# Kernel tuning notes

Measured on AMD Instinct MI355X. Metric: run time of the kernel, lower is better.

Reference implementation:

```python
import jax, jax.numpy as jnp
import numpy as np


def setup_inputs() -> dict:
    key = jax.random.key(0)
    ks = jax.random.split(key, 6)
    B, Q, K = 4, 512, 1024
    Dq, Dk, Dv, H = 512, 512, 512, 128
    return {
        "queries": jax.random.normal(ks[0], (B, Q, Dq), dtype=jnp.float32),
        "keys": jax.random.normal(ks[1], (B, K, Dk), dtype=jnp.float32),
        "values": jax.random.normal(ks[2], (B, K, Dv), dtype=jnp.float32),
        "W_q": jax.random.normal(ks[3], (Dq, H), dtype=jnp.float32) / np.sqrt(Dq),
        "W_k": jax.random.normal(ks[4], (Dk, H), dtype=jnp.float32) / np.sqrt(Dk),
        "w_v": jax.random.normal(ks[5], (H,), dtype=jnp.float32) / np.sqrt(H),
    }


def reference(queries, keys, values, W_q, W_k, w_v):
    # Additive (Bahdanau) attention.
    q = jnp.einsum("bqd,dh->bqh", queries, W_q)          # [B,Q,H]
    k = jnp.einsum("bkd,dh->bkh", keys, W_k)             # [B,K,H]
    features = jnp.tanh(q[:, :, None, :] + k[:, None, :, :])  # [B,Q,K,H]
    scores = jnp.einsum("bqkh,h->bqk", features, w_v)    # [B,Q,K]
    attn = jax.nn.softmax(scores, axis=-1)               # [B,Q,K]
    return jnp.einsum("bqk,bkv->bqv", attn, values)      # [B,Q,Dv]
```

## Files before the change

### kernel.cpp

```cpp
#include <hip/hip_runtime.h>

#define BB   4
#define QS   512
#define KSZ  1024
#define DD   512
#define HH   128
#define DVV  512

typedef unsigned int uint;
typedef unsigned short ushort;
typedef __attribute__((ext_vector_type(8)))  short short8;
typedef __attribute__((ext_vector_type(16))) float f32x16;

__device__ __forceinline__ float rcp_fast(float x)  { return __builtin_amdgcn_rcpf(x); }
__device__ __forceinline__ float exp2_fast(float x) { return __builtin_amdgcn_exp2f(x); }

__device__ __forceinline__ void split1(float v, ushort& h, ushort& l) {
    uint u = __float_as_uint(v);
    h = (ushort)(u >> 16);
    float r = v - __uint_as_float(u & 0xffff0000u);
    l = (ushort)(__float_as_uint(r) >> 16);
}

#define NSQ  (BB * QS * DD / 4 / 256)
#define NSK  (BB * KSZ * DD / 4 / 256)
#define NWT  128
#define NVT  (BB * (KSZ / 32) * (DVV / 32))

__global__ __launch_bounds__(256) void split_kernel(
    const float* __restrict__ q, const float* __restrict__ k,
    const float* __restrict__ Wq, const float* __restrict__ Wk,
    const float* __restrict__ val,
    ushort* __restrict__ qh, ushort* __restrict__ ql,
    ushort* __restrict__ kh, ushort* __restrict__ kl,
    ushort* __restrict__ wqh, ushort* __restrict__ wql,
    ushort* __restrict__ wkh, ushort* __restrict__ wkl,
    ushort* __restrict__ vhi, ushort* __restrict__ vlo)
{
    const int id  = blockIdx.x;
    const int tid = threadIdx.x;

    if (id < NSQ + NSK) {
        const float* src; ushort* dh; ushort* dl; size_t i;
        if (id < NSQ) { src = q; dh = qh; dl = ql; i = (size_t)id * 256 + tid; }
        else          { src = k; dh = kh; dl = kl; i = (size_t)(id - NSQ) * 256 + tid; }
        float4 v = ((const float4*)src)[i];
        ushort h0,h1,h2,h3,l0,l1,l2,l3;
        split1(v.x,h0,l0); split1(v.y,h1,l1); split1(v.z,h2,l2); split1(v.w,h3,l3);
        *(ushort4*)&dh[i * 4] = make_ushort4(h0,h1,h2,h3);
        *(ushort4*)&dl[i * 4] = make_ushort4(l0,l1,l2,l3);
        return;
    }
    if (id < NSQ + NSK + NWT) {
        __shared__ float Ts[32][33];
        int t = id - (NSQ + NSK);
        const float* W; ushort* dh; ushort* dl;
        if (t < 64) { W = Wq; dh = wqh; dl = wql; }
        else        { W = Wk; dh = wkh; dl = wkl; t -= 64; }
        const int d0 = (t >> 2) * 32, h0 = (t & 3) * 32;
        {
            const int dd = tid >> 3, c4 = (tid & 7) * 4;
            float4 v = *(const float4*)&W[(size_t)(d0 + dd) * HH + h0 + c4];
            Ts[dd][c4 + 0] = v.x; Ts[dd][c4 + 1] = v.y;
            Ts[dd][c4 + 2] = v.z; Ts[dd][c4 + 3] = v.w;
        }
        __syncthreads();
        {
            const int hh = tid >> 3, d4 = (tid & 7) * 4;
            ushort h[4], l[4];
            #pragma unroll
            for (int i = 0; i < 4; i++) split1(Ts[d4 + i][hh], h[i], l[i]);
            size_t o = (size_t)(h0 + hh) * DD + d0 + d4;
            *(ushort4*)&dh[o] = make_ushort4(h[0], h[1], h[2], h[3]);
            *(ushort4*)&dl[o] = make_ushort4(l[0], l[1], l[2], l[3]);
        }
        return;
    }
    {
        __shared__ float Ts[32][33];
        const int t   = id - (NSQ + NSK + NWT);
        const int b   = t >> 9;
        const int rem = t & 511;
        const int k0  = (rem >> 4) * 32;
        const int n0  = (rem & 15) * 32;
        {
            const int kk = tid >> 3, n4 = (tid & 7) * 4;
            float4 v = *(const float4*)&val[((size_t)b * KSZ + k0 + kk) * DVV + n0 + n4];
            Ts[kk][n4 + 0] = v.x; Ts[kk][n4 + 1] = v.y;
            Ts[kk][n4 + 2] = v.z; Ts[kk][n4 + 3] = v.w;
        }
        __syncthreads();
        {
            const int nn = tid >> 3, k4 = (tid & 7) * 4;
            ushort h[4], l[4];
            #pragma unroll
            for (int i = 0; i < 4; i++) split1(Ts[k4 + i][nn], h[i], l[i]);
            size_t o = ((size_t)b * DVV + n0 + nn) * KSZ + k0 + k4;
            *(ushort4*)&vhi[o] = make_ushort4(h[0], h[1], h[2], h[3]);
            *(ushort4*)&vlo[o] = make_ushort4(l[0], l[1], l[2], l[3]);
        }
    }
}

__global__ __launch_bounds__(256) void proj_mfma_kernel(
    const ushort* __restrict__ qh, const ushort* __restrict__ ql,
    const ushort* __restrict__ kh, const ushort* __restrict__ kl,
    const ushort* __restrict__ wqh, const ushort* __restrict__ wql,
    const ushort* __restrict__ wkh, const ushort* __restrict__ wkl,
    float* __restrict__ eq, float* __restrict__ ek)
{
    const int tid = threadIdx.x, w = tid >> 6, lane = tid & 63;
    const int row = lane & 31, kg = lane >> 5;
    const int gw = blockIdx.x * 4 + w;

    const ushort *pa_h, *pa_l, *pb_h, *pb_l; float* op; int m0, nt;
    if (gw < 256) {
        m0 = (gw >> 2) * 32; nt = gw & 3;
        pa_h = qh; pa_l = ql; pb_h = wqh; pb_l = wql; op = eq;
    } else {
        const int g = gw - 256;
        m0 = (g >> 2) * 32; nt = g & 3;
        pa_h = kh; pa_l = kl; pb_h = wkh; pb_l = wkl; op = ek;
    }

    const ushort* ah_p = pa_h + (size_t)(m0 + row) * DD + kg * 8;
    const ushort* al_p = pa_l + (size_t)(m0 + row) * DD + kg * 8;
    const ushort* bh_p = pb_h + (size_t)(nt * 32 + row) * DD + kg * 8;
    const ushort* bl_p = pb_l + (size_t)(nt * 32 + row) * DD + kg * 8;

    f32x16 acc;
    #pragma unroll
    for (int i = 0; i < 16; i++) acc[i] = 0.f;

    #pragma unroll 4
    for (int ks = 0; ks < DD; ks += 16) {
        short8 ah = *(const short8*)(ah_p + ks);
        short8 al = *(const short8*)(al_p + ks);
        short8 bh = *(const short8*)(bh_p + ks);
        short8 bl = *(const short8*)(bl_p + ks);
        acc = __builtin_amdgcn_mfma_f32_32x32x16_bf16(ah, bh, acc, 0, 0, 0);
        acc = __builtin_amdgcn_mfma_f32_32x32x16_bf16(ah, bl, acc, 0, 0, 0);
        acc = __builtin_amdgcn_mfma_f32_32x32x16_bf16(al, bh, acc, 0, 0, 0);
    }

    const float C2L = 2.8853900817779268f;
    float* ob = op + (size_t)m0 * HH + nt * 32;
    #pragma unroll
    for (int r = 0; r < 16; r++) {
        const int rb = (r & 3) + 8 * (r >> 2) + 4 * kg;
        ob[(size_t)rb * HH + row] = exp2_fast(acc[r] * C2L);
    }
}

__global__ __launch_bounds__(256) void scores_kernel(
    const float* __restrict__ eq, const float* __restrict__ ek,
    const float* __restrict__ wv, ushort* __restrict__ Phi,
    ushort* __restrict__ Plo, float* __restrict__ rsp)
{
    __shared__ float eqs[64][68];
    __shared__ float eks[64][68];

    const int tid = threadIdx.x;
    const int b  = blockIdx.z;
    const int q0 = blockIdx.y * 64;
    const int k0 = blockIdx.x * 64;

    const float* eqb = eq + ((size_t)b * QS  + q0) * HH;
    const float* ekb = ek + ((size_t)b * KSZ + k0) * HH;

    const int tk = tid & 15;
    const int tq = tid >> 4;

    float acc[4][4] = {};

    for (int hc = 0; hc < HH; hc += 64) {
        __syncthreads();
        #pragma unroll
        for (int i = 0; i < 4; i++) {
            int f = tid + i * 256;
            int row = f >> 4, c4 = f & 15;
            *(float4*)&eqs[row][c4 * 4] =
                *(const float4*)&eqb[(size_t)row * HH + hc + c4 * 4];
            *(float4*)&eks[row][c4 * 4] =
                *(const float4*)&ekb[(size_t)row * HH + hc + c4 * 4];
        }
        __syncthreads();

        for (int h0 = 0; h0 < 64; h0 += 4) {
            float4 wv4 = *(const float4*)&wv[hc + h0];
            float4 eq4[4], ek4[4];
            #pragma unroll
            for (int j = 0; j < 4; j++) {
                eq4[j] = *(const float4*)&eqs[tq + 16 * j][h0];
                ek4[j] = *(const float4*)&eks[tk + 16 * j][h0];
            }
            #pragma unroll
            for (int jq = 0; jq < 4; jq++) {
                #pragma unroll
                for (int jk = 0; jk < 4; jk++) {
                    float u0 = fminf(fmaf(eq4[jq].x, ek4[jk].x, 1.0f), 3e7f);
                    float u1 = fminf(fmaf(eq4[jq].y, ek4[jk].y, 1.0f), 3e7f);
                    float u2 = fminf(fmaf(eq4[jq].z, ek4[jk].z, 1.0f), 3e7f);
                    float u3 = fminf(fmaf(eq4[jq].w, ek4[jk].w, 1.0f), 3e7f);
                    float p01 = u0 * u1, p23 = u2 * u3;
                    float n01 = fmaf(wv4.x, u1, wv4.y * u0);
                    float n23 = fmaf(wv4.z, u3, wv4.w * u2);
                    float N = fmaf(n01, p23, n23 * p01);
                    acc[jq][jk] = fmaf(N, rcp_fast(p01 * p23), acc[jq][jk]);
                }
            }
        }
    }

    const float CN = -2.8853900817779268f;
    ushort* ph = Phi + ((size_t)b * QS + q0) * KSZ + k0;
    ushort* pl = Plo + ((size_t)b * QS + q0) * KSZ + k0;
    #pragma unroll
    for (int jq = 0; jq < 4; jq++) {
        float rowp = 0.f;
        #pragma unroll
        for (int jk = 0; jk < 4; jk++) {
            float pv_ = exp2_fast(acc[jq][jk] * CN);
            ushort hh, ll; split1(pv_, hh, ll);
            size_t o = (size_t)(tq + 16 * jq) * KSZ + tk + 16 * jk;
            ph[o] = hh; pl[o] = ll;
            rowp += pv_;
        }
        #pragma unroll
        for (int m = 8; m; m >>= 1) rowp += __shfl_xor(rowp, m);
        if ((tid & 15) == 0)
            rsp[((size_t)b * QS + q0 + tq + 16 * jq) * 16 + blockIdx.x] = rowp;
    }
}

__global__ __launch_bounds__(256) void pv_mfma_kernel(
    const ushort* __restrict__ Phi, const ushort* __restrict__ Plo,
    const ushort* __restrict__ vhi, const ushort* __restrict__ vlo,
    const float* __restrict__ rsp, float* __restrict__ outp)
{
    __shared__ float invs[32];
    __shared__ float accs[2][32][33];

    const int id  = blockIdx.x;
    const int x   = id & 7;
    const int j   = id >> 3;
    const int bm  = x * 8 + (j >> 3);
    const int ntp = j & 7;
    const int b   = bm >> 4, mt = bm & 15;

    const int tid = threadIdx.x, w = tid >> 6, lane = tid & 63;
    const int row = lane & 31, kg = lane >> 5;

    if (tid < 32) {
        const float* rp = rsp + ((size_t)b * QS + mt * 32 + tid) * 16;
        float s = 0.f;
        #pragma unroll
        for (int i = 0; i < 16; i++) s += rp[i];
        invs[tid] = rcp_fast(s);
    }

    const int nt  = ntp * 2 + (w >> 1);
    const int kh0 = (w & 1) * (KSZ / 2);

    const ushort* pah = Phi + ((size_t)b * QS  + mt * 32 + row) * KSZ + kh0 + kg * 8;
    const ushort* pal = Plo + ((size_t)b * QS  + mt * 32 + row) * KSZ + kh0 + kg * 8;
    const ushort* bhp = vhi + ((size_t)b * DVV + nt * 32 + row) * KSZ + kh0 + kg * 8;
    const ushort* blp = vlo + ((size_t)b * DVV + nt * 32 + row) * KSZ + kh0 + kg * 8;

    f32x16 acc;
    #pragma unroll
    for (int i = 0; i < 16; i++) acc[i] = 0.f;

    #pragma unroll 4
    for (int kb = 0; kb < KSZ / 2; kb += 16) {
        short8 ah = *(const short8*)(pah + kb);
        short8 al = *(const short8*)(pal + kb);
        short8 vh = *(const short8*)(bhp + kb);
        short8 vl = *(const short8*)(blp + kb);
        acc = __builtin_amdgcn_mfma_f32_32x32x16_bf16(ah, vh, acc, 0, 0, 0);
        acc = __builtin_amdgcn_mfma_f32_32x32x16_bf16(ah, vl, acc, 0, 0, 0);
        acc = __builtin_amdgcn_mfma_f32_32x32x16_bf16(al, vh, acc, 0, 0, 0);
    }

    if (w & 1) {
        #pragma unroll
        for (int r = 0; r < 16; r++)
            accs[w >> 1][(r & 3) + 8 * (r >> 2) + 4 * kg][row] = acc[r];
    }
    __syncthreads();
    if (!(w & 1)) {
        float* ob = outp + ((size_t)b * QS + mt * 32) * DVV + nt * 32;
        #pragma unroll
        for (int r = 0; r < 16; r++) {
            const int rb = (r & 3) + 8 * (r >> 2) + 4 * kg;
            float v = acc[r] + accs[w >> 1][rb][row];
            ob[(size_t)rb * DVV + row] = v * invs[rb];
        }
    }
}

extern "C" void kernel_launch(void* const* d_in, const int* in_sizes, int n_in,
                              void* d_out, int out_size, void* d_ws, size_t ws_size,
                              hipStream_t stream)
{
    const float* queries = (const float*)d_in[0];
    const float* keys    = (const float*)d_in[1];
    const float* values  = (const float*)d_in[2];
    const float* Wq      = (const float*)d_in[3];
    const float* Wk      = (const float*)d_in[4];
    const float* wv      = (const float*)d_in[5];
    float* out = (float*)d_out;

    float*  eq  = (float*)d_ws;
    float*  ek  = eq + (size_t)BB * QS * HH;
    float*  rsp = ek + (size_t)BB * KSZ * HH;
    ushort* Phi = (ushort*)(rsp + (size_t)BB * QS * 16);
    ushort* Plo = Phi + (size_t)BB * QS * KSZ;
    ushort* vhi = Plo + (size_t)BB * QS * KSZ;
    ushort* vlo = vhi + (size_t)BB * KSZ * DVV;
    ushort* qh  = vlo + (size_t)BB * KSZ * DVV;
    ushort* ql  = qh  + (size_t)BB * QS * DD;
    ushort* kh  = ql  + (size_t)BB * QS * DD;
    ushort* kl  = kh  + (size_t)BB * KSZ * DD;
    ushort* wqh = kl  + (size_t)BB * KSZ * DD;
    ushort* wql = wqh + (size_t)HH * DD;
    ushort* wkh = wql + (size_t)HH * DD;
    ushort* wkl = wkh + (size_t)HH * DD;

    split_kernel<<<dim3(NSQ + NSK + NWT + NVT), 256, 0, stream>>>(
        queries, keys, Wq, Wk, values,
        qh, ql, kh, kl, wqh, wql, wkh, wkl, vhi, vlo);

    proj_mfma_kernel<<<dim3(192), 256, 0, stream>>>(
        qh, ql, kh, kl, wqh, wql, wkh, wkl, eq, ek);

    scores_kernel<<<dim3(KSZ / 64, QS / 64, BB), 256, 0, stream>>>(
        eq, ek, wv, Phi, Plo, rsp);

    pv_mfma_kernel<<<dim3(512), 256, 0, stream>>>(Phi, Plo, vhi, vlo, rsp, out);
}
```

Measured before the change: 163.2 us.

## Move V transpose-split into projection kernel and dual-accumulate PV MFMA chain

The values transpose/split work moves out of the split kernel and into the projection kernel as extra blocks. This lets the memory-bound V conversion overlap with the MFMA projection and shortens the critical first kernel. The PV kernel now uses two independent accumulators to break the serial MFMA dependency chain, and the projection loop unroll rises to 8. The trade-offs are more registers and a mixed-workload kernel whose block types may be scheduled unevenly.

```diff
diff --git a/kernel.cpp b/kernel.cpp
--- a/kernel.cpp
+++ b/kernel.cpp
@@ -25,17 +25,16 @@
 #define NSQ  (BB * QS * DD / 4 / 256)
 #define NSK  (BB * KSZ * DD / 4 / 256)
 #define NWT  128
+#define NPJ  192
 #define NVT  (BB * (KSZ / 32) * (DVV / 32))
 
 __global__ __launch_bounds__(256) void split_kernel(
     const float* __restrict__ q, const float* __restrict__ k,
     const float* __restrict__ Wq, const float* __restrict__ Wk,
-    const float* __restrict__ val,
     ushort* __restrict__ qh, ushort* __restrict__ ql,
     ushort* __restrict__ kh, ushort* __restrict__ kl,
     ushort* __restrict__ wqh, ushort* __restrict__ wql,
-    ushort* __restrict__ wkh, ushort* __restrict__ wkl,
-    ushort* __restrict__ vhi, ushort* __restrict__ vlo)
+    ushort* __restrict__ wkh, ushort* __restrict__ wkl)
 {
     const int id  = blockIdx.x;
     const int tid = threadIdx.x;
@@ -51,34 +50,45 @@
         *(ushort4*)&dl[i * 4] = make_ushort4(l0,l1,l2,l3);
         return;
     }
-    if (id < NSQ + NSK + NWT) {
+    __shared__ float Ts[32][33];
+    int t = id - (NSQ + NSK);
+    const float* W; ushort* dh; ushort* dl;
+    if (t < 64) { W = Wq; dh = wqh; dl = wql; }
+    else        { W = Wk; dh = wkh; dl = wkl; t -= 64; }
+    const int d0 = (t >> 2) * 32, h0 = (t & 3) * 32;
+    {
+        const int dd = tid >> 3, c4 = (tid & 7) * 4;
+        float4 v = *(const float4*)&W[(size_t)(d0 + dd) * HH + h0 + c4];
+        Ts[dd][c4 + 0] = v.x; Ts[dd][c4 + 1] = v.y;
+        Ts[dd][c4 + 2] = v.z; Ts[dd][c4 + 3] = v.w;
+    }
+    __syncthreads();
+    {
+        const int hh = tid >> 3, d4 = (tid & 7) * 4;
+        ushort h[4], l[4];
+        #pragma unroll
+        for (int i = 0; i < 4; i++) split1(Ts[d4 + i][hh], h[i], l[i]);
+        size_t o = (size_t)(h0 + hh) * DD + d0 + d4;
+        *(ushort4*)&dh[o] = make_ushort4(h[0], h[1], h[2], h[3]);
+        *(ushort4*)&dl[o] = make_ushort4(l[0], l[1], l[2], l[3]);
+    }
+}
+
+__global__ __launch_bounds__(256) void projvt_kernel(
+    const ushort* __restrict__ qh, const ushort* __restrict__ ql,
+    const ushort* __restrict__ kh, const ushort* __restrict__ kl,
+    const ushort* __restrict__ wqh, const ushort* __restrict__ wql,
+    const ushort* __restrict__ wkh, const ushort* __restrict__ wkl,
+    const float* __restrict__ val,
+    float* __restrict__ eq, float* __restrict__ ek,
+    ushort* __restrict__ vhi, ushort* __restrict__ vlo)
+{
+    const int id  = blockIdx.x;
+    const int tid = threadIdx.x;
+
+    if (id >= NPJ) {
         __shared__ float Ts[32][33];
-        int t = id - (NSQ + NSK);
-        const float* W; ushort* dh; ushort* dl;
-        if (t < 64) { W = Wq; dh = wqh; dl = wql; }
-        else        { W = Wk; dh = wkh; dl = wkl; t -= 64; }
-        const int d0 = (t >> 2) * 32, h0 = (t & 3) * 32;
-        {
-            const int dd = tid >> 3, c4 = (tid & 7) * 4;
-            float4 v = *(const float4*)&W[(size_t)(d0 + dd) * HH + h0 + c4];
-            Ts[dd][c4 + 0] = v.x; Ts[dd][c4 + 1] = v.y;
-            Ts[dd][c4 + 2] = v.z; Ts[dd][c4 + 3] = v.w;
-        }
-        __syncthreads();
-        {
-            const int hh = tid >> 3, d4 = (tid & 7) * 4;
-            ushort h[4], l[4];
-            #pragma unroll
-            for (int i = 0; i < 4; i++) split1(Ts[d4 + i][hh], h[i], l[i]);
-            size_t o = (size_t)(h0 + hh) * DD + d0 + d4;
-            *(ushort4*)&dh[o] = make_ushort4(h[0], h[1], h[2], h[3]);
-            *(ushort4*)&dl[o] = make_ushort4(l[0], l[1], l[2], l[3]);
-        }
-        return;
-    }
-    {
-        __shared__ float Ts[32][33];
-        const int t   = id - (NSQ + NSK + NWT);
+        const int t   = id - NPJ;
         const int b   = t >> 9;
         const int rem = t & 511;
         const int k0  = (rem >> 4) * 32;
@@ -99,19 +109,12 @@
             *(ushort4*)&vhi[o] = make_ushort4(h[0], h[1], h[2], h[3]);
             *(ushort4*)&vlo[o] = make_ushort4(l[0], l[1], l[2], l[3]);
         }
-    }
-}
-
-__global__ __launch_bounds__(256) void proj_mfma_kernel(
-    const ushort* __restrict__ qh, const ushort* __restrict__ ql,
-    const ushort* __restrict__ kh, const ushort* __restrict__ kl,
-    const ushort* __restrict__ wqh, const ushort* __restrict__ wql,
-    const ushort* __restrict__ wkh, const ushort* __restrict__ wkl,
-    float* __restrict__ eq, float* __restrict__ ek)
-{
-    const int tid = threadIdx.x, w = tid >> 6, lane = tid & 63;
+        return;
+    }
+
+    const int w = tid >> 6, lane = tid & 63;
     const int row = lane & 31, kg = lane >> 5;
-    const int gw = blockIdx.x * 4 + w;
+    const int gw = id * 4 + w;
 
     const ushort *pa_h, *pa_l, *pb_h, *pb_l; float* op; int m0, nt;
     if (gw < 256) {
@@ -132,7 +135,7 @@
     #pragma unroll
     for (int i = 0; i < 16; i++) acc[i] = 0.f;
 
-    #pragma unroll 4
+    #pragma unroll 8
     for (int ks = 0; ks < DD; ks += 16) {
         short8 ah = *(const short8*)(ah_p + ks);
         short8 al = *(const short8*)(al_p + ks);
@@ -267,25 +270,34 @@
     const ushort* bhp = vhi + ((size_t)b * DVV + nt * 32 + row) * KSZ + kh0 + kg * 8;
     const ushort* blp = vlo + ((size_t)b * DVV + nt * 32 + row) * KSZ + kh0 + kg * 8;
 
-    f32x16 acc;
-    #pragma unroll
-    for (int i = 0; i < 16; i++) acc[i] = 0.f;
+    f32x16 acc0, acc1;
+    #pragma unroll
+    for (int i = 0; i < 16; i++) { acc0[i] = 0.f; acc1[i] = 0.f; }
 
     #pragma unroll 4
-    for (int kb = 0; kb < KSZ / 2; kb += 16) {
-        short8 ah = *(const short8*)(pah + kb);
-        short8 al = *(const short8*)(pal + kb);
-        short8 vh = *(const short8*)(bhp + kb);
-        short8 vl = *(const short8*)(blp + kb);
-        acc = __builtin_amdgcn_mfma_f32_32x32x16_bf16(ah, vh, acc, 0, 0, 0);
-        acc = __builtin_amdgcn_mfma_f32_32x32x16_bf16(ah, vl, acc, 0, 0, 0);
-        acc = __builtin_amdgcn_mfma_f32_32x32x16_bf16(al, vh, acc, 0, 0, 0);
-    }
+    for (int kb = 0; kb < KSZ / 2; kb += 32) {
+        short8 a0h = *(const short8*)(pah + kb);
+        short8 a0l = *(const short8*)(pal + kb);
+        short8 v0h = *(const short8*)(bhp + kb);
+        short8 v0l = *(const short8*)(blp + kb);
+        short8 a1h = *(const short8*)(pah + kb + 16);
+        short8 a1l = *(const short8*)(pal + kb + 16);
+        short8 v1h = *(const short8*)(bhp + kb + 16);
+        short8 v1l = *(const short8*)(blp + kb + 16);
+        acc0 = __builtin_amdgcn_mfma_f32_32x32x16_bf16(a0h, v0h, acc0, 0, 0, 0);
+        acc1 = __builtin_amdgcn_mfma_f32_32x32x16_bf16(a1h, v1h, acc1, 0, 0, 0);
+        acc0 = __builtin_amdgcn_mfma_f32_32x32x16_bf16(a0h, v0l, acc0, 0, 0, 0);
+        acc1 = __builtin_amdgcn_mfma_f32_32x32x16_bf16(a1h, v1l, acc1, 0, 0, 0);
+        acc0 = __builtin_amdgcn_mfma_f32_32x32x16_bf16(a0l, v0h, acc0, 0, 0, 0);
+        acc1 = __builtin_amdgcn_mfma_f32_32x32x16_bf16(a1l, v1h, acc1, 0, 0, 0);
+    }
+    #pragma unroll
+    for (int i = 0; i < 16; i++) acc0[i] += acc1[i];
 
     if (w & 1) {
         #pragma unroll
         for (int r = 0; r < 16; r++)
-            accs[w >> 1][(r & 3) + 8 * (r >> 2) + 4 * kg][row] = acc[r];
+            accs[w >> 1][(r & 3) + 8 * (r >> 2) + 4 * kg][row] = acc0[r];
     }
     __syncthreads();
     if (!(w & 1)) {
@@ -293,7 +305,7 @@
         #pragma unroll
         for (int r = 0; r < 16; r++) {
             const int rb = (r & 3) + 8 * (r >> 2) + 4 * kg;
-            float v = acc[r] + accs[w >> 1][rb][row];
+            float v = acc0[r] + accs[w >> 1][rb][row];
             ob[(size_t)rb * DVV + row] = v * invs[rb];
         }
     }
@@ -327,12 +339,11 @@
     ushort* wkh = wql + (size_t)HH * DD;
     ushort* wkl = wkh + (size_t)HH * DD;
 
-    split_kernel<<<dim3(NSQ + NSK + NWT + NVT), 256, 0, stream>>>(
-        queries, keys, Wq, Wk, values,
-        qh, ql, kh, kl, wqh, wql, wkh, wkl, vhi, vlo);
-
-    proj_mfma_kernel<<<dim3(192), 256, 0, stream>>>(
-        qh, ql, kh, kl, wqh, wql, wkh, wkl, eq, ek);
+    split_kernel<<<dim3(NSQ + NSK + NWT), 256, 0, stream>>>(
+        queries, keys, Wq, Wk, qh, ql, kh, kl, wqh, wql, wkh, wkl);
+
+    projvt_kernel<<<dim3(NPJ + NVT), 256, 0, stream>>>(
+        qh, ql, kh, kl, wqh, wql, wkh, wkl, values, eq, ek, vhi, vlo);
 
     scores_kernel<<<dim3(KSZ / 64, QS / 64, BB), 256, 0, stream>>>(
         eq, ek, wv, Phi, Plo, rsp);
```

Result: no change. 161.2 us (-1.2%).
